# Kernel tuning notes

Hardware: AMD Instinct MI355X
Metric: run time of the kernel (lower is better)

Reference implementation:

```python
import jax, jax.numpy as jnp
import numpy as np

D_MODEL = 1024
N_EXPERTS = 8
TOP_K = 2


def setup_inputs() -> dict:
    key = jax.random.key(0)
    ks = jax.random.split(key, 8)
    B, S, D, E, H = 4, 2048, D_MODEL, N_EXPERTS, 4 * D_MODEL
    s1 = 1.0 / np.sqrt(D)
    s2 = 1.0 / np.sqrt(H)
    return {
        "x": jax.random.normal(ks[0], (B, S, D), dtype=jnp.float32),
        "Wg": jax.random.uniform(ks[1], (D, E), jnp.float32, -s1, s1),
        "bg": jax.random.uniform(ks[2], (E,), jnp.float32, -s1, s1),
        "W1": jax.random.uniform(ks[3], (E, D, H), jnp.float32, -s1, s1),
        "b1": jax.random.uniform(ks[4], (E, H), jnp.float32, -s1, s1),
        "W2": jax.random.uniform(ks[5], (E, H, D), jnp.float32, -s2, s2),
        "b2": jax.random.uniform(ks[6], (E, D), jnp.float32, -s2, s2),
    }


def reference(x, Wg, bg, W1, b1, W2, b2):
    B, S, D = x.shape
    E = Wg.shape[1]
    x_flat = x.reshape(-1, D)                      # [T, D]
    logits = x_flat @ Wg + bg                      # [T, E]
    weights = jax.nn.softmax(logits, axis=-1)
    topk_w, topk_idx = jax.lax.top_k(weights, TOP_K)  # [T, K]
    # Per-token combine weight for each expert (sum over k where routed).
    onehot = jax.nn.one_hot(topk_idx, E, dtype=x.dtype)      # [T, K, E]
    combine = jnp.einsum("tk,tke->te", topk_w, onehot)       # [T, E]
    out = jnp.zeros_like(x_flat)
    for e in range(E):  # small fixed loop over experts
        h = jax.nn.gelu(x_flat @ W1[e] + b1[e], approximate=False)
        out = out + combine[:, e:e + 1] * (h @ W2[e] + b2[e])
    return out.reshape(B, S, D)
```

## Files before the change

### kernel.cpp

```cpp
#include <hip/hip_runtime.h>
#include <hip/hip_bf16.h>
#include <math.h>

#define T_TOK 8192
#define DM    1024
#define NE    8
#define HD    4096

typedef __bf16 bf16;
typedef __attribute__((ext_vector_type(8))) __bf16 bf16x8;
typedef __attribute__((ext_vector_type(4))) float  f32x4;

__device__ __forceinline__ void gl_lds16(const void* g, void* l) {
  __builtin_amdgcn_global_load_lds((const __attribute__((address_space(1))) void*)g,
                                   (__attribute__((address_space(3))) void*)l, 16, 0, 0);
}

#define RAW_BARRIER() asm volatile("s_barrier" ::: "memory")
#define VMCNT4()      asm volatile("s_waitcnt vmcnt(4)" ::: "memory")
#define LGKM0()       asm volatile("s_waitcnt lgkmcnt(0)" ::: "memory")

__device__ __forceinline__ int imin(int a, int b) { return a < b ? a : b; }

__global__ void zero_kernel(float* __restrict__ out, int* __restrict__ counts) {
  size_t stride = (size_t)gridDim.x * blockDim.x;
  size_t n4 = (size_t)T_TOK * DM / 4;
  for (size_t i = (size_t)blockIdx.x * blockDim.x + threadIdx.x; i < n4; i += stride) {
    float4 z = {0.f, 0.f, 0.f, 0.f};
    ((float4*)out)[i] = z;
  }
  if (blockIdx.x == 0 && threadIdx.x < NE) counts[threadIdx.x] = 0;
}

__global__ void transpose_cvt_kernel(const float* __restrict__ in, bf16* __restrict__ out,
                                     int R, int C) {
  __shared__ float tile[64][65];
  int e = blockIdx.z;
  int c0 = blockIdx.x * 64, r0 = blockIdx.y * 64;
  int tid = threadIdx.x;
  int lr = tid >> 2, lc = (tid & 3) * 16;
  const float* src = in + ((size_t)e * R + r0 + lr) * C + c0 + lc;
#pragma unroll
  for (int q = 0; q < 4; ++q) {
    float4 v = *(const float4*)(src + q * 4);
    tile[lr][lc + q * 4 + 0] = v.x;
    tile[lr][lc + q * 4 + 1] = v.y;
    tile[lr][lc + q * 4 + 2] = v.z;
    tile[lr][lc + q * 4 + 3] = v.w;
  }
  __syncthreads();
  int oc = tid >> 3;
  int rchunk = tid & 7;
#pragma unroll
  for (int q = 0; q < 2; ++q) {
    int ocq = oc + q * 32;
    bf16x8 o;
#pragma unroll
    for (int k = 0; k < 8; ++k) o[k] = (bf16)tile[rchunk * 8 + k][ocq];
    *(bf16x8*)(out + ((size_t)e * C + c0 + ocq) * R + r0 + rchunk * 8) = o;
  }
}

__global__ void gating_kernel(const float* __restrict__ x, const float* __restrict__ Wg,
                              const float* __restrict__ bg, int* __restrict__ counts,
                              int* __restrict__ tokl, float* __restrict__ wgt,
                              bf16* __restrict__ xb) {
  int t = blockIdx.x * 4 + (threadIdx.x >> 6);
  int lane = threadIdx.x & 63;
  if (t >= T_TOK) return;
  double acc[NE];
#pragma unroll
  for (int e = 0; e < NE; ++e) acc[e] = 0.0;
  const float* xr = x + (size_t)t * DM;
  bf16* xbr = xb + (size_t)t * DM;
  for (int d = lane; d < DM; d += 64) {
    float xv = xr[d];
    xbr[d] = (bf16)xv;
#pragma unroll
    for (int e = 0; e < NE; ++e) acc[e] += (double)xv * (double)Wg[d * NE + e];
  }
#pragma unroll
  for (int e = 0; e < NE; ++e)
    for (int o = 32; o > 0; o >>= 1) acc[e] += __shfl_down(acc[e], o, 64);
  if (lane == 0) {
    float l[NE], w[NE];
    float m = -1e30f;
#pragma unroll
    for (int e = 0; e < NE; ++e) { l[e] = (float)acc[e] + bg[e]; m = fmaxf(m, l[e]); }
    float s = 0.f;
#pragma unroll
    for (int e = 0; e < NE; ++e) { w[e] = expf(l[e] - m); s += w[e]; }
    float inv = 1.f / s;
#pragma unroll
    for (int e = 0; e < NE; ++e) w[e] *= inv;
    int e1 = 0; float v1 = w[0];
#pragma unroll
    for (int e = 1; e < NE; ++e) if (w[e] > v1) { v1 = w[e]; e1 = e; }
    int e2 = -1; float v2 = -1.f;
#pragma unroll
    for (int e = 0; e < NE; ++e) if (e != e1 && w[e] > v2) { v2 = w[e]; e2 = e; }
    int s1 = atomicAdd(&counts[e1], 1);
    tokl[e1 * T_TOK + s1] = t; wgt[e1 * T_TOK + s1] = v1;
    int s2 = atomicAdd(&counts[e2], 1);
    tokl[e2 * T_TOK + s2] = t; wgt[e2 * T_TOK + s2] = v2;
  }
}

__global__ void scan_kernel(const int* __restrict__ counts, int* __restrict__ offsets) {
  if (threadIdx.x == 0 && blockIdx.x == 0) {
    int s = 0;
#pragma unroll
    for (int e = 0; e < NE; ++e) { offsets[e] = s; s += counts[e]; }
    offsets[NE] = s;
  }
}


#define LDA_F(IH, CB) \
  _Pragma("unroll") for (int kh = 0; kh < 2; ++kh) \
  _Pragma("unroll") for (int i = 0; i < 4; ++i) \
    af[kh*4+i] = *(const bf16x8*)(Ab + (CB) + (128*(IH) + 64*wm + 16*i + lf) * 128 + (colx ^ (kh*64)));

#define LDB_F(JH, CB) \
  _Pragma("unroll") for (int kh = 0; kh < 2; ++kh) \
  _Pragma("unroll") for (int j = 0; j < 2; ++j) \
    bfr[kh*2+j] = *(const bf16x8*)(Bb + (CB) + (128*(JH) + 32*wn + 16*j + lf) * 128 + (colx ^ (kh*64)));

#define MM_F(IH, JH) \
  _Pragma("unroll") for (int kh = 0; kh < 2; ++kh) \
  _Pragma("unroll") for (int i = 0; i < 4; ++i) \
  _Pragma("unroll") for (int j = 0; j < 2; ++j) \
    acc[IH][JH][i][j] = __builtin_amdgcn_mfma_f32_16x16x32_bf16(af[kh*4+i], bfr[kh*2+j], acc[IH][JH][i][j], 0, 0, 0);

#define ISSUE_A(H, NBO, KB) do { \
    gl_lds16(gA[2*(H)] + (KB), Al + (NBO) + (H)*16384 + dst); \
    gl_lds16(gA[2*(H)+1] + (KB), Al + (NBO) + (H)*16384 + 8192 + dst); \
  } while (0)
#define ISSUE_B(H, NBO, KB) do { \
    gl_lds16(gB[2*(H)] + (KB), Bl + (NBO) + (H)*16384 + dst); \
    gl_lds16(gB[2*(H)+1] + (KB), Bl + (NBO) + (H)*16384 + 8192 + dst); \
  } while (0)

#define PH_TAIL(IH, JH) \
    RAW_BARRIER(); \
    LGKM0(); __builtin_amdgcn_sched_barrier(0); \
    __builtin_amdgcn_s_setprio(1); \
    MM_F(IH, JH); \
    __builtin_amdgcn_s_setprio(0);

#define KTILE_BODY(CB, NBO, KB) \
     \
    LDA_F(0, CB); \
    LDB_F(0, CB); \
    ISSUE_A(0, NBO, KB); \
    PH_TAIL(0, 0) \
    VMCNT4(); \
    RAW_BARRIER(); \
     \
    LDB_F(1, CB); \
    ISSUE_B(0, NBO, KB); \
    PH_TAIL(0, 1) \
    VMCNT4(); \
    RAW_BARRIER(); \
     \
    LDA_F(1, CB); \
    LDB_F(0, CB); \
    ISSUE_B(1, NBO, KB); \
    PH_TAIL(1, 0) \
    RAW_BARRIER(); \
     \
    LDB_F(1, CB); \
    ISSUE_A(1, NBO, KB); \
    PH_TAIL(1, 1) \
    VMCNT4(); \
    RAW_BARRIER();

__global__ __launch_bounds__(512, 2) void gemm1_kernel(
    const bf16* __restrict__ xbf, const bf16* __restrict__ w1t,
    const float* __restrict__ b1, const int* __restrict__ counts,
    const int* __restrict__ offsets, const int* __restrict__ tokl,
    bf16* __restrict__ hbuf, int Hc, int cbase) {
  int bid = blockIdx.x;
  int q = gridDim.x >> 3;
  int L = (bid & 7) * q + (bid >> 3);
  int rt = L & 31;
  int g = L >> 5;
  int NT = Hc >> 8;
  int nt = g % NT, e = g / NT;
  int cnt = counts[e];
  if (rt * 256 >= cnt) return;
  __shared__ __align__(16) bf16 sA[2][256 * 64];
  __shared__ __align__(16) bf16 sB[2][256 * 64];
  int tid = threadIdx.x, lane = tid & 63, w = tid >> 6;
  int wm = w & 1, wn = w >> 1;
  int lf = lane & 15;
  int colx = ((lane >> 4) * 16) ^ ((lane & 7) << 4);
  int ra = tid >> 3;
  int ko = (tid & 7) * 16;
  int kox = ko ^ ((ra & 7) << 4);
  int dst = w * 1024;
  int hoff = offsets[e];
  const char* gA[4];
  const char* gB[4];
#pragma unroll
  for (int s = 0; s < 4; ++s) {
    int r = imin(rt * 256 + ra + s * 64, cnt - 1);
    int t = tokl[e * T_TOK + r];
    gA[s] = (const char*)(xbf + (size_t)t * DM) + kox;
    int col = cbase + nt * 256 + ra + s * 64;
    gB[s] = (const char*)(w1t + ((size_t)e * HD + col) * DM) + kox;
  }
  char* Al = (char*)sA;
  char* Bl = (char*)sB;
  const char* Ab = (const char*)sA;
  const char* Bb = (const char*)sB;
  f32x4 acc[2][2][4][2];
#pragma unroll
  for (int ih = 0; ih < 2; ++ih)
#pragma unroll
    for (int jh = 0; jh < 2; ++jh)
#pragma unroll
      for (int i = 0; i < 4; ++i)
#pragma unroll
        for (int j = 0; j < 2; ++j) acc[ih][jh][i][j] = {0.f, 0.f, 0.f, 0.f};
  bf16x8 af[8], bfr[4];
  const int K = DM / 64;
  ISSUE_A(0, 0, 0); ISSUE_B(0, 0, 0); ISSUE_B(1, 0, 0); ISSUE_A(1, 0, 0);
  VMCNT4();
  RAW_BARRIER();
  for (int k = 0; k < K; ++k) {
    int cb = (k & 1) * 32768;
    int nbo = ((k + 1) & 1) * 32768;
    int kb = (k + 1 < K) ? (k + 1) * 128 : 0;
    KTILE_BODY(cb, nbo, kb)
  }
  int colq = lane & 15, rowq = (lane >> 4) * 4;
  size_t ebase = (size_t)e * HD + cbase + nt * 256;
  float b1v[2][2];
#pragma unroll
  for (int jh = 0; jh < 2; ++jh)
#pragma unroll
    for (int j = 0; j < 2; ++j)
      b1v[jh][j] = b1[ebase + 128 * jh + 32 * wn + 16 * j + colq];
#pragma unroll
  for (int ih = 0; ih < 2; ++ih) {
#pragma unroll
    for (int i = 0; i < 4; ++i) {
#pragma unroll
      for (int r = 0; r < 4; ++r) {
        int grow = rt * 256 + 128 * ih + 64 * wm + 16 * i + rowq + r;
        if (grow < cnt) {
          size_t hrow = (size_t)(hoff + grow) * Hc + nt * 256;
#pragma unroll
          for (int jh = 0; jh < 2; ++jh) {
#pragma unroll
            for (int j = 0; j < 2; ++j) {
              float v = acc[ih][jh][i][j][r] + b1v[jh][j];
              float gl = 0.5f * v * (1.f + erff(v * 0.70710678118654752f));
              hbuf[hrow + 128 * jh + 32 * wn + 16 * j + colq] = (bf16)gl;
            }
          }
        }
      }
    }
  }
}

__global__ __launch_bounds__(512, 2) void gemm2_kernel(
    const bf16* __restrict__ hbuf, const bf16* __restrict__ w2t,
    const float* __restrict__ b2, const int* __restrict__ counts,
    const int* __restrict__ offsets, const int* __restrict__ tokl,
    const float* __restrict__ wgt, float* __restrict__ out,
    int Hc, int cbase, float b2scale) {
  int bid = blockIdx.x;
  int q = gridDim.x >> 3;
  int L = (bid & 7) * q + (bid >> 3);
  int rt = L & 31;
  int g = L >> 5;
  const int NT = DM / 256;
  int nt = g % NT, e = g / NT;
  int cnt = counts[e];
  if (rt * 256 >= cnt) return;
  __shared__ __align__(16) bf16 sA[2][256 * 64];
  __shared__ __align__(16) bf16 sB[2][256 * 64];
  int tid = threadIdx.x, lane = tid & 63, w = tid >> 6;
  int wm = w & 1, wn = w >> 1;
  int lf = lane & 15;
  int colx = ((lane >> 4) * 16) ^ ((lane & 7) << 4);
  int ra = tid >> 3;
  int ko = (tid & 7) * 16;
  int kox = ko ^ ((ra & 7) << 4);
  int dst = w * 1024;
  int hoff = offsets[e];
  const char* gA[4];
  const char* gB[4];
#pragma unroll
  for (int s = 0; s < 4; ++s) {
    int r = imin(rt * 256 + ra + s * 64, cnt - 1);
    gA[s] = (const char*)(hbuf + (size_t)(hoff + r) * Hc) + kox;
    int col = nt * 256 + ra + s * 64;
    gB[s] = (const char*)(w2t + ((size_t)e * DM + col) * HD + cbase) + kox;
  }
  char* Al = (char*)sA;
  char* Bl = (char*)sB;
  const char* Ab = (const char*)sA;
  const char* Bb = (const char*)sB;
  f32x4 acc[2][2][4][2];
#pragma unroll
  for (int ih = 0; ih < 2; ++ih)
#pragma unroll
    for (int jh = 0; jh < 2; ++jh)
#pragma unroll
      for (int i = 0; i < 4; ++i)
#pragma unroll
        for (int j = 0; j < 2; ++j) acc[ih][jh][i][j] = {0.f, 0.f, 0.f, 0.f};
  bf16x8 af[8], bfr[4];
  const int K = Hc / 64;
  ISSUE_A(0, 0, 0); ISSUE_B(0, 0, 0); ISSUE_B(1, 0, 0); ISSUE_A(1, 0, 0);
  VMCNT4();
  RAW_BARRIER();
  for (int k = 0; k < K; ++k) {
    int cb = (k & 1) * 32768;
    int nbo = ((k + 1) & 1) * 32768;
    int kb = (k + 1 < K) ? (k + 1) * 128 : 0;
    KTILE_BODY(cb, nbo, kb)
  }
  int colq = lane & 15, rowq = (lane >> 4) * 4;
  float b2v[2][2];
#pragma unroll
  for (int jh = 0; jh < 2; ++jh)
#pragma unroll
    for (int j = 0; j < 2; ++j)
      b2v[jh][j] = b2[(size_t)e * DM + nt * 256 + 128 * jh + 32 * wn + 16 * j + colq] * b2scale;
#pragma unroll
  for (int ih = 0; ih < 2; ++ih) {
#pragma unroll
    for (int i = 0; i < 4; ++i) {
#pragma unroll
      for (int r = 0; r < 4; ++r) {
        int grow = rt * 256 + 128 * ih + 64 * wm + 16 * i + rowq + r;
        if (grow < cnt) {
          float wv = wgt[e * T_TOK + grow];
          int tk = tokl[e * T_TOK + grow];
          float* orow = out + (size_t)tk * DM + nt * 256;
#pragma unroll
          for (int jh = 0; jh < 2; ++jh) {
#pragma unroll
            for (int j = 0; j < 2; ++j)
              atomicAdd(orow + 128 * jh + 32 * wn + 16 * j + colq,
                        wv * (acc[ih][jh][i][j][r] + b2v[jh][j]));
          }
        }
      }
    }
  }
}

extern "C" void kernel_launch(void* const* d_in, const int* in_sizes, int n_in,
                              void* d_out, int out_size, void* d_ws, size_t ws_size,
                              hipStream_t stream) {
  const float* x  = (const float*)d_in[0];
  const float* Wg = (const float*)d_in[1];
  const float* bg = (const float*)d_in[2];
  const float* W1 = (const float*)d_in[3];
  const float* b1 = (const float*)d_in[4];
  const float* W2 = (const float*)d_in[5];
  const float* b2 = (const float*)d_in[6];
  float* out = (float*)d_out;

  char* ws = (char*)d_ws;
  size_t off = 0;
  auto alloc = [&](size_t bytes) -> void* {
    void* p = ws + off;
    off = (off + bytes + 255) & ~(size_t)255;
    return p;
  };
  int*   counts  = (int*)alloc(NE * 4);
  int*   offsets = (int*)alloc((NE + 1) * 4);
  int*   tokl    = (int*)alloc((size_t)NE * T_TOK * 4);
  float* wgt     = (float*)alloc((size_t)NE * T_TOK * 4);
  bf16*  xbf     = (bf16*)alloc((size_t)T_TOK * DM * 2);
  bf16*  w1t     = (bf16*)alloc((size_t)NE * HD * DM * 2);
  bf16*  w2t     = (bf16*)alloc((size_t)NE * DM * HD * 2);
  size_t remain = ws_size > off ? ws_size - off : 0;
  int Hc = HD;
  while (Hc > 256 && (size_t)2 * T_TOK * Hc * 2 > remain) Hc >>= 1;
  bf16* hbuf = (bf16*)alloc((size_t)2 * T_TOK * Hc * 2);

  zero_kernel<<<4096, 256, 0, stream>>>(out, counts);
  transpose_cvt_kernel<<<dim3(HD / 64, DM / 64, NE), 256, 0, stream>>>(W1, w1t, DM, HD);
  transpose_cvt_kernel<<<dim3(DM / 64, HD / 64, NE), 256, 0, stream>>>(W2, w2t, HD, DM);
  gating_kernel<<<T_TOK / 4, 256, 0, stream>>>(x, Wg, bg, counts, tokl, wgt, xbf);
  scan_kernel<<<1, 64, 0, stream>>>(counts, offsets);

  int nchunk = HD / Hc;
  for (int c = 0; c < nchunk; ++c) {
    gemm1_kernel<<<NE * (Hc / 256) * (T_TOK / 256), 512, 0, stream>>>(
        xbf, w1t, b1, counts, offsets, tokl, hbuf, Hc, c * Hc);
    gemm2_kernel<<<NE * (DM / 256) * (T_TOK / 256), 512, 0, stream>>>(
        hbuf, w2t, b2, counts, offsets, tokl, wgt, out, Hc, c * Hc, c == 0 ? 1.f : 0.f);
  }
}
```

Baseline: 1.112 ms.

## Restructure GEMM k-tile pipeline into two phases with both B fragments held

The four-phase k-tile loop, with a barrier and lgkmcnt wait before each MFMA block, becomes two phases. Both B fragment halves are now kept in registers (bfr0/bfr1), so each A half is multiplied against both B halves. This halves the number of barriers and regroups the global-to-LDS prefetch issues and vmcnt waits to match. In exchange it uses more VGPRs for the extra B fragments, which may pressure occupancy under launch_bounds(512,2). It also drops the explicit lgkmcnt(0) and sched_barrier, leaving LDS read ordering to the compiler.

```diff
diff --git a/kernel.cpp b/kernel.cpp
--- a/kernel.cpp
+++ b/kernel.cpp
@@ -17,8 +17,8 @@
 }
 
 #define RAW_BARRIER() asm volatile("s_barrier" ::: "memory")
-#define VMCNT4()      asm volatile("s_waitcnt vmcnt(4)" ::: "memory")
-#define LGKM0()       asm volatile("s_waitcnt lgkmcnt(0)" ::: "memory")
+#define VMCNT6()      asm volatile("s_waitcnt vmcnt(6)" ::: "memory")
+#define VMCNT2()      asm volatile("s_waitcnt vmcnt(2)" ::: "memory")
 
 __device__ __forceinline__ int imin(int a, int b) { return a < b ? a : b; }
 
@@ -121,16 +121,16 @@
   _Pragma("unroll") for (int i = 0; i < 4; ++i) \
     af[kh*4+i] = *(const bf16x8*)(Ab + (CB) + (128*(IH) + 64*wm + 16*i + lf) * 128 + (colx ^ (kh*64)));
 
-#define LDB_F(JH, CB) \
+#define LDB_F(BF, JH, CB) \
   _Pragma("unroll") for (int kh = 0; kh < 2; ++kh) \
   _Pragma("unroll") for (int j = 0; j < 2; ++j) \
-    bfr[kh*2+j] = *(const bf16x8*)(Bb + (CB) + (128*(JH) + 32*wn + 16*j + lf) * 128 + (colx ^ (kh*64)));
-
-#define MM_F(IH, JH) \
+    BF[kh*2+j] = *(const bf16x8*)(Bb + (CB) + (128*(JH) + 32*wn + 16*j + lf) * 128 + (colx ^ (kh*64)));
+
+#define MM_F(IH, JH, BF) \
   _Pragma("unroll") for (int kh = 0; kh < 2; ++kh) \
   _Pragma("unroll") for (int i = 0; i < 4; ++i) \
   _Pragma("unroll") for (int j = 0; j < 2; ++j) \
-    acc[IH][JH][i][j] = __builtin_amdgcn_mfma_f32_16x16x32_bf16(af[kh*4+i], bfr[kh*2+j], acc[IH][JH][i][j], 0, 0, 0);
+    acc[IH][JH][i][j] = __builtin_amdgcn_mfma_f32_16x16x32_bf16(af[kh*4+i], BF[kh*2+j], acc[IH][JH][i][j], 0, 0, 0);
 
 #define ISSUE_A(H, NBO, KB) do { \
     gl_lds16(gA[2*(H)] + (KB), Al + (NBO) + (H)*16384 + dst); \
@@ -141,38 +141,30 @@
     gl_lds16(gB[2*(H)+1] + (KB), Bl + (NBO) + (H)*16384 + 8192 + dst); \
   } while (0)
 
-#define PH_TAIL(IH, JH) \
-    RAW_BARRIER(); \
-    LGKM0(); __builtin_amdgcn_sched_barrier(0); \
-    __builtin_amdgcn_s_setprio(1); \
-    MM_F(IH, JH); \
-    __builtin_amdgcn_s_setprio(0);
-
 #define KTILE_BODY(CB, NBO, KB) \
      \
     LDA_F(0, CB); \
-    LDB_F(0, CB); \
+    LDB_F(bfr0, 0, CB); \
+    LDB_F(bfr1, 1, CB); \
     ISSUE_A(0, NBO, KB); \
-    PH_TAIL(0, 0) \
-    VMCNT4(); \
+    ISSUE_B(0, NBO, KB); \
+    ISSUE_B(1, NBO, KB); \
+    VMCNT6(); \
     RAW_BARRIER(); \
-     \
-    LDB_F(1, CB); \
-    ISSUE_B(0, NBO, KB); \
-    PH_TAIL(0, 1) \
-    VMCNT4(); \
+    __builtin_amdgcn_s_setprio(1); \
+    MM_F(0, 0, bfr0); \
+    MM_F(0, 1, bfr1); \
+    __builtin_amdgcn_s_setprio(0); \
     RAW_BARRIER(); \
      \
     LDA_F(1, CB); \
-    LDB_F(0, CB); \
-    ISSUE_B(1, NBO, KB); \
-    PH_TAIL(1, 0) \
+    ISSUE_A(1, NBO, KB); \
+    VMCNT2(); \
     RAW_BARRIER(); \
-     \
-    LDB_F(1, CB); \
-    ISSUE_A(1, NBO, KB); \
-    PH_TAIL(1, 1) \
-    VMCNT4(); \
+    __builtin_amdgcn_s_setprio(1); \
+    MM_F(1, 0, bfr0); \
+    MM_F(1, 1, bfr1); \
+    __builtin_amdgcn_s_setprio(0); \
     RAW_BARRIER();
 
 __global__ __launch_bounds__(512, 2) void gemm1_kernel(
@@ -223,10 +215,10 @@
       for (int i = 0; i < 4; ++i)
 #pragma unroll
         for (int j = 0; j < 2; ++j) acc[ih][jh][i][j] = {0.f, 0.f, 0.f, 0.f};
-  bf16x8 af[8], bfr[4];
+  bf16x8 af[8], bfr0[4], bfr1[4];
   const int K = DM / 64;
   ISSUE_A(0, 0, 0); ISSUE_B(0, 0, 0); ISSUE_B(1, 0, 0); ISSUE_A(1, 0, 0);
-  VMCNT4();
+  VMCNT2();
   RAW_BARRIER();
   for (int k = 0; k < K; ++k) {
     int cb = (k & 1) * 32768;
@@ -314,10 +306,10 @@
       for (int i = 0; i < 4; ++i)
 #pragma unroll
         for (int j = 0; j < 2; ++j) acc[ih][jh][i][j] = {0.f, 0.f, 0.f, 0.f};
-  bf16x8 af[8], bfr[4];
+  bf16x8 af[8], bfr0[4], bfr1[4];
   const int K = Hc / 64;
   ISSUE_A(0, 0, 0); ISSUE_B(0, 0, 0); ISSUE_B(1, 0, 0); ISSUE_A(1, 0, 0);
-  VMCNT4();
+  VMCNT2();
   RAW_BARRIER();
   for (int k = 0; k < K; ++k) {
     int cb = (k & 1) * 32768;
```

After: 1.103 ms. About the same (-0.8%).
